# Performance work log

Measured on AMD Instinct MI355X. Metric: run time of the kernel, lower is better.

Reference implementation:

```python
import jax, jax.numpy as jnp
import numpy as np

N_NODES = 200000  # graph size
D = 128           # feature dim == out_size
N1 = 81920        # layer-1 node set size
B = 8192          # batch size
K = 10            # num_sample neighbors


def setup_inputs() -> dict:
    key = jax.random.key(0)
    k = jax.random.split(key, 7)
    raw_features = jax.random.normal(k[0], (N_NODES, D), dtype=jnp.float32)
    # xavier-like scale for weights [out, 2*in]
    W1 = jax.random.normal(k[1], (D, 2 * D), dtype=jnp.float32) * (1.0 / np.sqrt(2 * D))
    W2 = jax.random.normal(k[2], (D, 2 * D), dtype=jnp.float32) * (1.0 / np.sqrt(2 * D))
    layer1_nodes = jax.random.randint(k[3], (N1,), 0, N_NODES)
    neigh0_idx = jax.random.randint(k[4], (N1, K), 0, N_NODES)
    map_batch = jax.random.randint(k[5], (B,), 0, N1)
    neigh1_idx = jax.random.randint(k[6], (B, K), 0, N1)
    return {
        "raw_features": raw_features,
        "W1": W1,
        "W2": W2,
        "layer1_nodes": layer1_nodes,
        "neigh0_idx": neigh0_idx,
        "map_batch": map_batch,
        "neigh1_idx": neigh1_idx,
    }


def _sage_layer(self_feats, agg_feats, W):
    # combined = cat([self, agg], dim=1); relu(W @ combined.T).T == relu(combined @ W.T)
    combined = jnp.concatenate([self_feats, agg_feats], axis=1)
    return jax.nn.relu(combined @ W.T)


def reference(raw_features, W1, W2, layer1_nodes, neigh0_idx, map_batch, neigh1_idx):
    # Layer 1: aggregate raw features over K sampled neighbors (MEAN), gcn=False
    agg0 = jnp.mean(raw_features[neigh0_idx], axis=1)        # [N1, D]
    self0 = raw_features[layer1_nodes]                        # [N1, D]
    h1 = _sage_layer(self0, agg0, W1)                         # [N1, D]
    # Layer 2: aggregate layer-1 embeddings for the batch nodes
    agg1 = jnp.mean(h1[neigh1_idx], axis=1)                   # [B, D]
    self1 = h1[map_batch]                                     # [B, D]
    h2 = _sage_layer(self1, agg1, W2)                         # [B, D]
    return h2
```

## Files before the change

### kernel.cpp

```cpp
#include <hip/hip_runtime.h>
#include <stdint.h>

#define D 128
#define K_NEI 10
#define TILE_M 64

typedef __bf16 bf16x8 __attribute__((ext_vector_type(8)));
typedef float f32x4 __attribute__((ext_vector_type(4)));

__device__ __forceinline__ uint32_t f2bf(float f) {
    union { float f; uint32_t u; } v; v.f = f;
    uint32_t u = v.u;
    return (u + 0x7FFFu + ((u >> 16) & 1u)) >> 16;
}
__device__ __forceinline__ float bf2f(uint32_t h) {
    union { uint32_t u; float f; } v; v.u = h << 16; return v.f;
}
__device__ __forceinline__ uint32_t pack2(float a, float b) {
    return f2bf(a) | (f2bf(b) << 16);
}
__device__ __forceinline__ bf16x8 u4_as_bf16x8(uint4 u) {
    union { uint4 u; bf16x8 b; } v; v.u = u; return v.b;
}

__device__ __forceinline__ uint2 cvt4(f32x4 v) {
    union { __bf16 b[4]; uint2 u; } o;
    o.b[0] = (__bf16)v[0]; o.b[1] = (__bf16)v[1];
    o.b[2] = (__bf16)v[2]; o.b[3] = (__bf16)v[3];
    return o.u;
}
__device__ __forceinline__ bf16x8 cvt8(f32x4 lo, f32x4 hi) {
    union { __bf16 b[8]; bf16x8 v; } o;
    o.b[0] = (__bf16)lo[0]; o.b[1] = (__bf16)lo[1];
    o.b[2] = (__bf16)lo[2]; o.b[3] = (__bf16)lo[3];
    o.b[4] = (__bf16)hi[0]; o.b[5] = (__bf16)hi[1];
    o.b[6] = (__bf16)hi[2]; o.b[7] = (__bf16)hi[3];
    return o.v;
}

__global__ void convert_W2(const float* __restrict__ Wa, const float* __restrict__ Wb_in,
                           uint16_t* __restrict__ Oa, uint16_t* __restrict__ Ob)
{
    const float* W = (blockIdx.x < 16) ? Wa : Wb_in;
    uint16_t*    O = (blockIdx.x < 16) ? Oa : Ob;
    int t = (blockIdx.x & 15) * 256 + threadIdx.x;
    int c = t >> 4, j = t & 15;
    const float* src = W + (size_t)(c & 127) * 256 + (c >> 7) * 128 + j * 8;
    f32x4 a = *(const f32x4*)src;
    f32x4 b = *(const f32x4*)(src + 4);
    uint4 o;
    o.x = pack2(a[0], a[1]); o.y = pack2(a[2], a[3]);
    o.z = pack2(b[0], b[1]); o.w = pack2(b[2], b[3]);
    *(uint4*)(O + (size_t)c * 128 + j * 8) = o;
}

template <bool A_F32>
__global__ __launch_bounds__(256, 2)
void gemm_rw(const void* __restrict__ Asrc_,
             const uint16_t* __restrict__ Wb,
             uint16_t* __restrict__ P, int M)
{
    const int tid  = threadIdx.x;
    const int wave = tid >> 6;
    const int lane = tid & 63;
    const int r16  = lane & 15;
    const int q    = lane >> 4;
    const int h    = wave & 1;

    const int nTiles = M >> 4;
    const int stride = gridDim.x * 2;
    int tile = blockIdx.x * 2 + (wave >> 1);
    if (tile >= nTiles) return;

    bf16x8 Bf[8][4];
    {
        const uint16_t* wb = Wb + (size_t)(h * 128 + r16) * 128 + q * 8;
        #pragma unroll
        for (int nt = 0; nt < 8; ++nt)
            #pragma unroll
            for (int ks = 0; ks < 4; ++ks)
                Bf[nt][ks] = *(const bf16x8*)(wb + nt * 16 * 128 + ks * 32);
    }

    f32x4 preF[8];  uint4 preB[4];

    if (A_F32) {
        const float* row = (const float*)Asrc_ + (size_t)(tile * 16 + r16) * D + q * 8;
        #pragma unroll
        for (int ks = 0; ks < 4; ++ks) {
            preF[2 * ks]     = *(const f32x4*)(row + ks * 32);
            preF[2 * ks + 1] = *(const f32x4*)(row + ks * 32 + 4);
        }
    } else {
        const uint16_t* row = (const uint16_t*)Asrc_ + (size_t)(tile * 16 + r16) * D + q * 8;
        #pragma unroll
        for (int ks = 0; ks < 4; ++ks)
            preB[ks] = *(const uint4*)(row + ks * 32);
    }

    while (tile < nTiles) {
        const int nxt = tile + stride;

        bf16x8 a[4];
        if (A_F32) {
            #pragma unroll
            for (int ks = 0; ks < 4; ++ks)
                a[ks] = cvt8(preF[2 * ks], preF[2 * ks + 1]);
        } else {
            #pragma unroll
            for (int ks = 0; ks < 4; ++ks) a[ks] = u4_as_bf16x8(preB[ks]);
        }

        if (nxt < nTiles) {
            if (A_F32) {
                const float* row = (const float*)Asrc_ + (size_t)(nxt * 16 + r16) * D + q * 8;
                #pragma unroll
                for (int ks = 0; ks < 4; ++ks) {
                    preF[2 * ks]     = *(const f32x4*)(row + ks * 32);
                    preF[2 * ks + 1] = *(const f32x4*)(row + ks * 32 + 4);
                }
            } else {
                const uint16_t* row = (const uint16_t*)Asrc_ + (size_t)(nxt * 16 + r16) * D + q * 8;
                #pragma unroll
                for (int ks = 0; ks < 4; ++ks)
                    preB[ks] = *(const uint4*)(row + ks * 32);
            }
        }

        f32x4 acc[8];
        #pragma unroll
        for (int nt = 0; nt < 8; ++nt) acc[nt] = (f32x4){0.f, 0.f, 0.f, 0.f};

        #pragma unroll
        for (int ks = 0; ks < 4; ++ks)
            #pragma unroll
            for (int nt = 0; nt < 8; ++nt)
                acc[nt] = __builtin_amdgcn_mfma_f32_16x16x32_bf16(Bf[nt][ks], a[ks], acc[nt], 0, 0, 0);

        uint16_t* dst = P + (size_t)(tile * 16 + r16) * 256 + h * 128 + q * 4;
        #pragma unroll
        for (int nt = 0; nt < 8; ++nt)
            *(uint2*)(dst + nt * 16) = cvt4(acc[nt]);

        tile = nxt;
    }
}

template <bool OUT_F32>
__global__ void combine(const uint16_t* __restrict__ P,
                        const int* __restrict__ self_idx,
                        const int* __restrict__ neigh_idx,
                        void* __restrict__ out_, int M)
{
    const int t = blockIdx.x * 256 + threadIdx.x;
    const int i = t >> 4;
    const int j = t & 15;
    if (i >= M) return;

    uint4 sv = *(const uint4*)(P + (size_t)self_idx[i] * 256 + j * 8);

    const int2* nrow2 = (const int2*)(neigh_idx + (size_t)i * K_NEI);
    int idx[K_NEI];
    #pragma unroll
    for (int k = 0; k < 5; ++k) {
        int2 p = nrow2[k];
        idx[2 * k] = p.x; idx[2 * k + 1] = p.y;
    }

    float s0=0,s1=0,s2=0,s3=0,s4=0,s5=0,s6=0,s7=0;
    #pragma unroll
    for (int k = 0; k < K_NEI; ++k) {
        uint4 v = *(const uint4*)(P + (size_t)idx[k] * 256 + 128 + j * 8);
        s0 += bf2f(v.x & 0xFFFFu); s1 += bf2f(v.x >> 16);
        s2 += bf2f(v.y & 0xFFFFu); s3 += bf2f(v.y >> 16);
        s4 += bf2f(v.z & 0xFFFFu); s5 += bf2f(v.z >> 16);
        s6 += bf2f(v.w & 0xFFFFu); s7 += bf2f(v.w >> 16);
    }
    const float inv = 0.1f;
    float r0 = bf2f(sv.x & 0xFFFFu) + s0 * inv, r1 = bf2f(sv.x >> 16) + s1 * inv;
    float r2 = bf2f(sv.y & 0xFFFFu) + s2 * inv, r3 = bf2f(sv.y >> 16) + s3 * inv;
    float r4 = bf2f(sv.z & 0xFFFFu) + s4 * inv, r5 = bf2f(sv.z >> 16) + s5 * inv;
    float r6 = bf2f(sv.w & 0xFFFFu) + s6 * inv, r7 = bf2f(sv.w >> 16) + s7 * inv;
    r0 = r0 > 0.f ? r0 : 0.f; r1 = r1 > 0.f ? r1 : 0.f;
    r2 = r2 > 0.f ? r2 : 0.f; r3 = r3 > 0.f ? r3 : 0.f;
    r4 = r4 > 0.f ? r4 : 0.f; r5 = r5 > 0.f ? r5 : 0.f;
    r6 = r6 > 0.f ? r6 : 0.f; r7 = r7 > 0.f ? r7 : 0.f;

    if (OUT_F32) {
        float* dst = (float*)out_ + (size_t)i * D + j * 8;
        *(f32x4*)dst       = (f32x4){r0, r1, r2, r3};
        *(f32x4*)(dst + 4) = (f32x4){r4, r5, r6, r7};
    } else {
        uint4 o;
        o.x = pack2(r0, r1); o.y = pack2(r2, r3);
        o.z = pack2(r4, r5); o.w = pack2(r6, r7);
        *(uint4*)((uint16_t*)out_ + (size_t)i * D + j * 8) = o;
    }
}

template <bool FEATS_F32, bool OUT_F32>
__global__ void sage_layer(const void* __restrict__ feats_,
                           const float* __restrict__ W,
                           const int* __restrict__ self_idx,
                           const int* __restrict__ neigh_idx,
                           void* __restrict__ out_)
{
    __shared__ __align__(16) uint16_t Alds[TILE_M * 128];
    __shared__ __align__(16) uint16_t Wlds[128 * 128];

    const int tid  = threadIdx.x;
    const int wave = tid >> 6;
    const int lane = tid & 63;
    const int r16  = lane & 15;
    const int q    = lane >> 4;
    const int G    = blockIdx.x * TILE_M;

    const float*    feats_f = (const float*)feats_;
    const uint16_t* feats_b = (const uint16_t*)feats_;

    f32x4 acc[8];
    #pragma unroll
    for (int nt = 0; nt < 8; ++nt) acc[nt] = (f32x4){0.f, 0.f, 0.f, 0.f};

    for (int half = 0; half < 2; ++half) {
        #pragma unroll
        for (int it = 0; it < 8; ++it) {
            int t = it * 256 + tid;
            int j = t >> 4, c = t & 15;
            const float* src = W + (size_t)j * 256 + half * 128 + c * 8;
            f32x4 w0 = *(const f32x4*)(src);
            f32x4 w1 = *(const f32x4*)(src + 4);
            uint4 o;
            o.x = pack2(w0[0], w0[1]); o.y = pack2(w0[2], w0[3]);
            o.z = pack2(w1[0], w1[1]); o.w = pack2(w1[2], w1[3]);
            int cs = c ^ (j & 15);
            *(uint4*)(Wlds + j * 128 + cs * 8) = o;
        }
        if (half == 0) {
            #pragma unroll
            for (int it = 0; it < 4; ++it) {
                int t = it * 256 + tid;
                int n = t >> 4, c = t & 15;
                int node = self_idx[G + n];
                uint4 o;
                if (FEATS_F32) {
                    const float* src = feats_f + (size_t)node * D + c * 8;
                    f32x4 f0 = *(const f32x4*)(src);
                    f32x4 f1 = *(const f32x4*)(src + 4);
                    o.x = pack2(f0[0], f0[1]); o.y = pack2(f0[2], f0[3]);
                    o.z = pack2(f1[0], f1[1]); o.w = pack2(f1[2], f1[3]);
                } else {
                    o = *(const uint4*)(feats_b + (size_t)node * D + c * 8);
                }
                int cs = c ^ (n & 15);
                *(uint4*)(Alds + n * 128 + cs * 8) = o;
            }
        } else {
            #pragma unroll
            for (int it = 0; it < 4; ++it) {
                int t = it * 256 + tid;
                int n = t >> 4, c = t & 15;
                const int* nrow = neigh_idx + (size_t)(G + n) * K_NEI;
                float s0=0,s1=0,s2=0,s3=0,s4=0,s5=0,s6=0,s7=0;
                #pragma unroll
                for (int k = 0; k < K_NEI; ++k) {
                    if (FEATS_F32) {
                        const float* src = feats_f + (size_t)nrow[k] * D + c * 8;
                        f32x4 f0 = *(const f32x4*)(src);
                        f32x4 f1 = *(const f32x4*)(src + 4);
                        s0 += f0[0]; s1 += f0[1]; s2 += f0[2]; s3 += f0[3];
                        s4 += f1[0]; s5 += f1[1]; s6 += f1[2]; s7 += f1[3];
                    } else {
                        uint4 v = *(const uint4*)(feats_b + (size_t)nrow[k] * D + c * 8);
                        s0 += bf2f(v.x & 0xFFFFu); s1 += bf2f(v.x >> 16);
                        s2 += bf2f(v.y & 0xFFFFu); s3 += bf2f(v.y >> 16);
                        s4 += bf2f(v.z & 0xFFFFu); s5 += bf2f(v.z >> 16);
                        s6 += bf2f(v.w & 0xFFFFu); s7 += bf2f(v.w >> 16);
                    }
                }
                const float inv = 0.1f;
                uint4 o;
                o.x = pack2(s0 * inv, s1 * inv);
                o.y = pack2(s2 * inv, s3 * inv);
                o.z = pack2(s4 * inv, s5 * inv);
                o.w = pack2(s6 * inv, s7 * inv);
                int cs = c ^ (n & 15);
                *(uint4*)(Alds + n * 128 + cs * 8) = o;
            }
        }
        __syncthreads();

        #pragma unroll
        for (int ks = 0; ks < 4; ++ks) {
            int cidx = ks * 4 + q;
            bf16x8 a = *(const bf16x8*)(Alds + (wave * 16 + r16) * 128 + ((cidx ^ r16) * 8));
            bf16x8 b[8];
            #pragma unroll
            for (int nt = 0; nt < 8; ++nt) {
                int jj = nt * 16 + r16;
                b[nt] = *(const bf16x8*)(Wlds + jj * 128 + ((cidx ^ r16) * 8));
            }
            #pragma unroll
            for (int nt = 0; nt < 8; ++nt)
                acc[nt] = __builtin_amdgcn_mfma_f32_16x16x32_bf16(a, b[nt], acc[nt], 0, 0, 0);
        }
        __syncthreads();
    }

    const int row_base = G + wave * 16 + q * 4;
    #pragma unroll
    for (int nt = 0; nt < 8; ++nt) {
        int col = nt * 16 + r16;
        #pragma unroll
        for (int r = 0; r < 4; ++r) {
            float v = acc[nt][r];
            v = v > 0.f ? v : 0.f;
            if (OUT_F32) ((float*)out_)[(size_t)(row_base + r) * D + col] = v;
            else ((uint16_t*)out_)[(size_t)(row_base + r) * D + col] = (uint16_t)f2bf(v);
        }
    }
}

extern "C" void kernel_launch(void* const* d_in, const int* in_sizes, int n_in,
                              void* d_out, int out_size, void* d_ws, size_t ws_size,
                              hipStream_t stream) {
    const float* raw = (const float*)d_in[0];
    const float* W1  = (const float*)d_in[1];
    const float* W2  = (const float*)d_in[2];
    const int* layer1_nodes = (const int*)d_in[3];
    const int* neigh0       = (const int*)d_in[4];
    const int* map_batch    = (const int*)d_in[5];
    const int* neigh1       = (const int*)d_in[6];

    const int N_NODES = in_sizes[0] / D;
    const int N1 = in_sizes[3];
    const int B  = in_sizes[5];

    const size_t szP  = (size_t)N_NODES * 256 * 2;
    const size_t szQ  = (size_t)N1 * 256 * 2;
    const size_t szH1 = (size_t)N1 * 128 * 2;
    const size_t szW  = 256 * 128 * 2;
    const size_t needA = (szP > szQ ? szP : szQ) + szH1 + 2 * szW;

    if (ws_size >= needA && (N_NODES % 16) == 0 && (N1 % 16) == 0 && (B % 16) == 0) {
        uint16_t* Pbuf = (uint16_t*)d_ws;
        uint16_t* h1   = (uint16_t*)((char*)d_ws + (szP > szQ ? szP : szQ));
        uint16_t* W1b  = h1 + (size_t)N1 * 128;
        uint16_t* W2b  = W1b + 256 * 128;

        convert_W2<<<32, 256, 0, stream>>>(W1, W2, W1b, W2b);

        gemm_rw<true ><<<512, 256, 0, stream>>>(raw, W1b, Pbuf, N_NODES);

        combine<false><<<(N1 * 16 + 255) / 256, 256, 0, stream>>>(Pbuf, layer1_nodes, neigh0, h1, N1);

        gemm_rw<false><<<512, 256, 0, stream>>>(h1, W2b, Pbuf, N1);

        combine<true ><<<(B * 16 + 255) / 256, 256, 0, stream>>>(Pbuf, map_batch, neigh1, d_out, B);
        return;
    }

    uint16_t* h1 = (uint16_t*)d_ws;
    sage_layer<true,  false><<<N1 / TILE_M, 256, 0, stream>>>(raw, W1, layer1_nodes, neigh0, h1);
    sage_layer<false, true ><<<B  / TILE_M, 256, 0, stream>>>(h1,  W2, map_batch,    neigh1, d_out);
}
```

Before: 251.4 us.

## Gather-then-GEMM: aggregate raw features before projecting instead of projecting all nodes

Replaces the project-all-nodes-then-gather scheme with gather-first. For each layer a gather kernel builds a concatenated [self, mean-neighbor] bf16 row, then a K=256 MFMA GEMM with fused ReLU produces the layer output. This removes the GEMM over all 200k graph nodes and its large intermediate write, which was mostly wasted because only about 81,920 rows are needed. In exchange, the layer-1 gather reads fp32 raw rows, which costs more bytes per gathered row, and it writes an extra concatenated buffer.

```diff
diff --git a/kernel.cpp b/kernel.cpp
--- a/kernel.cpp
+++ b/kernel.cpp
@@ -22,43 +22,92 @@
 __device__ __forceinline__ bf16x8 u4_as_bf16x8(uint4 u) {
     union { uint4 u; bf16x8 b; } v; v.u = u; return v.b;
 }
-
 __device__ __forceinline__ uint2 cvt4(f32x4 v) {
     union { __bf16 b[4]; uint2 u; } o;
     o.b[0] = (__bf16)v[0]; o.b[1] = (__bf16)v[1];
     o.b[2] = (__bf16)v[2]; o.b[3] = (__bf16)v[3];
     return o.u;
 }
-__device__ __forceinline__ bf16x8 cvt8(f32x4 lo, f32x4 hi) {
-    union { __bf16 b[8]; bf16x8 v; } o;
-    o.b[0] = (__bf16)lo[0]; o.b[1] = (__bf16)lo[1];
-    o.b[2] = (__bf16)lo[2]; o.b[3] = (__bf16)lo[3];
-    o.b[4] = (__bf16)hi[0]; o.b[5] = (__bf16)hi[1];
-    o.b[6] = (__bf16)hi[2]; o.b[7] = (__bf16)hi[3];
-    return o.v;
-}
-
-__global__ void convert_W2(const float* __restrict__ Wa, const float* __restrict__ Wb_in,
-                           uint16_t* __restrict__ Oa, uint16_t* __restrict__ Ob)
+
+__global__ void convert_Wc(const float* __restrict__ W1, const float* __restrict__ W2,
+                           uint16_t* __restrict__ O1, uint16_t* __restrict__ O2)
 {
-    const float* W = (blockIdx.x < 16) ? Wa : Wb_in;
-    uint16_t*    O = (blockIdx.x < 16) ? Oa : Ob;
+    const float* W = (blockIdx.x < 16) ? W1 : W2;
+    uint16_t*    O = (blockIdx.x < 16) ? O1 : O2;
     int t = (blockIdx.x & 15) * 256 + threadIdx.x;
-    int c = t >> 4, j = t & 15;
-    const float* src = W + (size_t)(c & 127) * 256 + (c >> 7) * 128 + j * 8;
+    const float* src = W + (size_t)t * 8;
     f32x4 a = *(const f32x4*)src;
     f32x4 b = *(const f32x4*)(src + 4);
     uint4 o;
-    o.x = pack2(a[0], a[1]); o.y = pack2(a[2], a[3]);
-    o.z = pack2(b[0], b[1]); o.w = pack2(b[2], b[3]);
-    *(uint4*)(O + (size_t)c * 128 + j * 8) = o;
-}
-
-template <bool A_F32>
-__global__ __launch_bounds__(256, 2)
-void gemm_rw(const void* __restrict__ Asrc_,
-             const uint16_t* __restrict__ Wb,
-             uint16_t* __restrict__ P, int M)
+    o.x = cvt4(a).x; o.y = cvt4(a).y;
+    o.z = cvt4(b).x; o.w = cvt4(b).y;
+    *(uint4*)(O + (size_t)t * 8) = o;
+}
+
+template <bool SRC_F32>
+__global__ void gather_agg(const void* __restrict__ src_,
+                           const int* __restrict__ self_idx,
+                           const int* __restrict__ neigh_idx,
+                           uint16_t* __restrict__ C, int M)
+{
+    const int t = blockIdx.x * 256 + threadIdx.x;
+    const int i = t >> 4;
+    const int j = t & 15;
+    if (i >= M) return;
+
+    const int2* nrow2 = (const int2*)(neigh_idx + (size_t)i * K_NEI);
+    int idx[K_NEI];
+    #pragma unroll
+    for (int k = 0; k < 5; ++k) {
+        int2 p = nrow2[k];
+        idx[2 * k] = p.x; idx[2 * k + 1] = p.y;
+    }
+    const int self = self_idx[i];
+    uint16_t* c = C + (size_t)i * 256;
+
+    if (SRC_F32) {
+        const float* src = (const float*)src_;
+        const float* srow = src + (size_t)self * D;
+        f32x4 sv0 = *(const f32x4*)(srow + j * 4);
+        f32x4 sv1 = *(const f32x4*)(srow + 64 + j * 4);
+        f32x4 s0 = (f32x4){0.f,0.f,0.f,0.f};
+        f32x4 s1 = (f32x4){0.f,0.f,0.f,0.f};
+        #pragma unroll
+        for (int k = 0; k < K_NEI; ++k) {
+            const float* r = src + (size_t)idx[k] * D;
+            s0 += *(const f32x4*)(r + j * 4);
+            s1 += *(const f32x4*)(r + 64 + j * 4);
+        }
+        *(uint2*)(c + j * 4)       = cvt4(sv0);
+        *(uint2*)(c + 64 + j * 4)  = cvt4(sv1);
+        *(uint2*)(c + 128 + j * 4) = cvt4(s0 * 0.1f);
+        *(uint2*)(c + 192 + j * 4) = cvt4(s1 * 0.1f);
+    } else {
+        const uint16_t* src = (const uint16_t*)src_;
+        uint4 sv = *(const uint4*)(src + (size_t)self * D + j * 8);
+        float s0=0,s1=0,s2=0,s3=0,s4=0,s5=0,s6=0,s7=0;
+        #pragma unroll
+        for (int k = 0; k < K_NEI; ++k) {
+            uint4 v = *(const uint4*)(src + (size_t)idx[k] * D + j * 8);
+            s0 += bf2f(v.x & 0xFFFFu); s1 += bf2f(v.x >> 16);
+            s2 += bf2f(v.y & 0xFFFFu); s3 += bf2f(v.y >> 16);
+            s4 += bf2f(v.z & 0xFFFFu); s5 += bf2f(v.z >> 16);
+            s6 += bf2f(v.w & 0xFFFFu); s7 += bf2f(v.w >> 16);
+        }
+        *(uint4*)(c + j * 8) = sv;
+        const float inv = 0.1f;
+        uint4 o;
+        o.x = pack2(s0 * inv, s1 * inv); o.y = pack2(s2 * inv, s3 * inv);
+        o.z = pack2(s4 * inv, s5 * inv); o.w = pack2(s6 * inv, s7 * inv);
+        *(uint4*)(c + 128 + j * 8) = o;
+    }
+}
+
+template <bool OUT_F32>
+__global__ __launch_bounds__(256)
+void gemm_k256(const uint16_t* __restrict__ A,
+               const uint16_t* __restrict__ Wc,
+               void* __restrict__ out_, int M)
 {
     const int tid  = threadIdx.x;
     const int wave = tid >> 6;
@@ -72,129 +121,61 @@
     int tile = blockIdx.x * 2 + (wave >> 1);
     if (tile >= nTiles) return;
 
-    bf16x8 Bf[8][4];
+    bf16x8 Wf[4][8];
     {
-        const uint16_t* wb = Wb + (size_t)(h * 128 + r16) * 128 + q * 8;
-        #pragma unroll
-        for (int nt = 0; nt < 8; ++nt)
-            #pragma unroll
-            for (int ks = 0; ks < 4; ++ks)
-                Bf[nt][ks] = *(const bf16x8*)(wb + nt * 16 * 128 + ks * 32);
-    }
-
-    f32x4 preF[8];  uint4 preB[4];
-
-    if (A_F32) {
-        const float* row = (const float*)Asrc_ + (size_t)(tile * 16 + r16) * D + q * 8;
-        #pragma unroll
-        for (int ks = 0; ks < 4; ++ks) {
-            preF[2 * ks]     = *(const f32x4*)(row + ks * 32);
-            preF[2 * ks + 1] = *(const f32x4*)(row + ks * 32 + 4);
-        }
-    } else {
-        const uint16_t* row = (const uint16_t*)Asrc_ + (size_t)(tile * 16 + r16) * D + q * 8;
-        #pragma unroll
-        for (int ks = 0; ks < 4; ++ks)
-            preB[ks] = *(const uint4*)(row + ks * 32);
+        const uint16_t* wb = Wc + (size_t)(h * 64 + r16) * 256 + q * 8;
+        #pragma unroll
+        for (int nt = 0; nt < 4; ++nt)
+            #pragma unroll
+            for (int ks = 0; ks < 8; ++ks)
+                Wf[nt][ks] = *(const bf16x8*)(wb + nt * 16 * 256 + ks * 32);
+    }
+
+    uint4 preB[8];
+    {
+        const uint16_t* row = A + (size_t)(tile * 16 + r16) * 256 + q * 8;
+        #pragma unroll
+        for (int ks = 0; ks < 8; ++ks) preB[ks] = *(const uint4*)(row + ks * 32);
     }
 
     while (tile < nTiles) {
         const int nxt = tile + stride;
 
-        bf16x8 a[4];
-        if (A_F32) {
-            #pragma unroll
-            for (int ks = 0; ks < 4; ++ks)
-                a[ks] = cvt8(preF[2 * ks], preF[2 * ks + 1]);
-        } else {
-            #pragma unroll
-            for (int ks = 0; ks < 4; ++ks) a[ks] = u4_as_bf16x8(preB[ks]);
-        }
+        bf16x8 a[8];
+        #pragma unroll
+        for (int ks = 0; ks < 8; ++ks) a[ks] = u4_as_bf16x8(preB[ks]);
 
         if (nxt < nTiles) {
-            if (A_F32) {
-                const float* row = (const float*)Asrc_ + (size_t)(nxt * 16 + r16) * D + q * 8;
-                #pragma unroll
-                for (int ks = 0; ks < 4; ++ks) {
-                    preF[2 * ks]     = *(const f32x4*)(row + ks * 32);
-                    preF[2 * ks + 1] = *(const f32x4*)(row + ks * 32 + 4);
-                }
-            } else {
-                const uint16_t* row = (const uint16_t*)Asrc_ + (size_t)(nxt * 16 + r16) * D + q * 8;
-                #pragma unroll
-                for (int ks = 0; ks < 4; ++ks)
-                    preB[ks] = *(const uint4*)(row + ks * 32);
-            }
-        }
-
-        f32x4 acc[8];
-        #pragma unroll
-        for (int nt = 0; nt < 8; ++nt) acc[nt] = (f32x4){0.f, 0.f, 0.f, 0.f};
-
-        #pragma unroll
-        for (int ks = 0; ks < 4; ++ks)
-            #pragma unroll
-            for (int nt = 0; nt < 8; ++nt)
-                acc[nt] = __builtin_amdgcn_mfma_f32_16x16x32_bf16(Bf[nt][ks], a[ks], acc[nt], 0, 0, 0);
-
-        uint16_t* dst = P + (size_t)(tile * 16 + r16) * 256 + h * 128 + q * 4;
-        #pragma unroll
-        for (int nt = 0; nt < 8; ++nt)
-            *(uint2*)(dst + nt * 16) = cvt4(acc[nt]);
-
+            const uint16_t* row = A + (size_t)(nxt * 16 + r16) * 256 + q * 8;
+            #pragma unroll
+            for (int ks = 0; ks < 8; ++ks) preB[ks] = *(const uint4*)(row + ks * 32);
+        }
+
+        f32x4 acc[4];
+        #pragma unroll
+        for (int nt = 0; nt < 4; ++nt) acc[nt] = (f32x4){0.f,0.f,0.f,0.f};
+
+        #pragma unroll
+        for (int ks = 0; ks < 8; ++ks)
+            #pragma unroll
+            for (int nt = 0; nt < 4; ++nt)
+                acc[nt] = __builtin_amdgcn_mfma_f32_16x16x32_bf16(Wf[nt][ks], a[ks], acc[nt], 0, 0, 0);
+
+        const size_t row = (size_t)(tile * 16 + r16);
+        const int col0 = h * 64 + q * 4;
+        #pragma unroll
+        for (int nt = 0; nt < 4; ++nt) {
+            f32x4 v = acc[nt];
+            v[0] = v[0] > 0.f ? v[0] : 0.f;
+            v[1] = v[1] > 0.f ? v[1] : 0.f;
+            v[2] = v[2] > 0.f ? v[2] : 0.f;
+            v[3] = v[3] > 0.f ? v[3] : 0.f;
+            if (OUT_F32)
+                *(f32x4*)((float*)out_ + row * 128 + col0 + nt * 16) = v;
+            else
+                *(uint2*)((uint16_t*)out_ + row * 128 + col0 + nt * 16) = cvt4(v);
+        }
         tile = nxt;
-    }
-}
-
-template <bool OUT_F32>
-__global__ void combine(const uint16_t* __restrict__ P,
-                        const int* __restrict__ self_idx,
-                        const int* __restrict__ neigh_idx,
-                        void* __restrict__ out_, int M)
-{
-    const int t = blockIdx.x * 256 + threadIdx.x;
-    const int i = t >> 4;
-    const int j = t & 15;
-    if (i >= M) return;
-
-    uint4 sv = *(const uint4*)(P + (size_t)self_idx[i] * 256 + j * 8);
-
-    const int2* nrow2 = (const int2*)(neigh_idx + (size_t)i * K_NEI);
-    int idx[K_NEI];
-    #pragma unroll
-    for (int k = 0; k < 5; ++k) {
-        int2 p = nrow2[k];
-        idx[2 * k] = p.x; idx[2 * k + 1] = p.y;
-    }
-
-    float s0=0,s1=0,s2=0,s3=0,s4=0,s5=0,s6=0,s7=0;
-    #pragma unroll
-    for (int k = 0; k < K_NEI; ++k) {
-        uint4 v = *(const uint4*)(P + (size_t)idx[k] * 256 + 128 + j * 8);
-        s0 += bf2f(v.x & 0xFFFFu); s1 += bf2f(v.x >> 16);
-        s2 += bf2f(v.y & 0xFFFFu); s3 += bf2f(v.y >> 16);
-        s4 += bf2f(v.z & 0xFFFFu); s5 += bf2f(v.z >> 16);
-        s6 += bf2f(v.w & 0xFFFFu); s7 += bf2f(v.w >> 16);
-    }
-    const float inv = 0.1f;
-    float r0 = bf2f(sv.x & 0xFFFFu) + s0 * inv, r1 = bf2f(sv.x >> 16) + s1 * inv;
-    float r2 = bf2f(sv.y & 0xFFFFu) + s2 * inv, r3 = bf2f(sv.y >> 16) + s3 * inv;
-    float r4 = bf2f(sv.z & 0xFFFFu) + s4 * inv, r5 = bf2f(sv.z >> 16) + s5 * inv;
-    float r6 = bf2f(sv.w & 0xFFFFu) + s6 * inv, r7 = bf2f(sv.w >> 16) + s7 * inv;
-    r0 = r0 > 0.f ? r0 : 0.f; r1 = r1 > 0.f ? r1 : 0.f;
-    r2 = r2 > 0.f ? r2 : 0.f; r3 = r3 > 0.f ? r3 : 0.f;
-    r4 = r4 > 0.f ? r4 : 0.f; r5 = r5 > 0.f ? r5 : 0.f;
-    r6 = r6 > 0.f ? r6 : 0.f; r7 = r7 > 0.f ? r7 : 0.f;
-
-    if (OUT_F32) {
-        float* dst = (float*)out_ + (size_t)i * D + j * 8;
-        *(f32x4*)dst       = (f32x4){r0, r1, r2, r3};
-        *(f32x4*)(dst + 4) = (f32x4){r4, r5, r6, r7};
-    } else {
-        uint4 o;
-        o.x = pack2(r0, r1); o.y = pack2(r2, r3);
-        o.z = pack2(r4, r5); o.w = pack2(r6, r7);
-        *(uint4*)((uint16_t*)out_ + (size_t)i * D + j * 8) = o;
     }
 }
 
@@ -332,31 +313,33 @@
     const int* map_batch    = (const int*)d_in[5];
     const int* neigh1       = (const int*)d_in[6];
 
-    const int N_NODES = in_sizes[0] / D;
     const int N1 = in_sizes[3];
     const int B  = in_sizes[5];
 
-    const size_t szP  = (size_t)N_NODES * 256 * 2;
-    const size_t szQ  = (size_t)N1 * 256 * 2;
+    const size_t szC1 = (size_t)N1 * 256 * 2;
     const size_t szH1 = (size_t)N1 * 128 * 2;
-    const size_t szW  = 256 * 128 * 2;
-    const size_t needA = (szP > szQ ? szP : szQ) + szH1 + 2 * szW;
-
-    if (ws_size >= needA && (N_NODES % 16) == 0 && (N1 % 16) == 0 && (B % 16) == 0) {
-        uint16_t* Pbuf = (uint16_t*)d_ws;
-        uint16_t* h1   = (uint16_t*)((char*)d_ws + (szP > szQ ? szP : szQ));
-        uint16_t* W1b  = h1 + (size_t)N1 * 128;
-        uint16_t* W2b  = W1b + 256 * 128;
-
-        convert_W2<<<32, 256, 0, stream>>>(W1, W2, W1b, W2b);
-
-        gemm_rw<true ><<<512, 256, 0, stream>>>(raw, W1b, Pbuf, N_NODES);
-
-        combine<false><<<(N1 * 16 + 255) / 256, 256, 0, stream>>>(Pbuf, layer1_nodes, neigh0, h1, N1);
-
-        gemm_rw<false><<<512, 256, 0, stream>>>(h1, W2b, Pbuf, N1);
-
-        combine<true ><<<(B * 16 + 255) / 256, 256, 0, stream>>>(Pbuf, map_batch, neigh1, d_out, B);
+    const size_t szC2 = (size_t)B * 256 * 2;
+    const size_t szW  = 128 * 256 * 2;
+    const size_t need = szC1 + szH1 + szC2 + 2 * szW;
+
+    if (ws_size >= need && (N1 % 16) == 0 && (B % 16) == 0) {
+        uint16_t* C1  = (uint16_t*)d_ws;
+        uint16_t* h1  = C1 + (size_t)N1 * 256;
+        uint16_t* C2  = h1 + (size_t)N1 * 128;
+        uint16_t* W1c = C2 + (size_t)B * 256;
+        uint16_t* W2c = W1c + 128 * 256;
+
+        convert_Wc<<<32, 256, 0, stream>>>(W1, W2, W1c, W2c);
+
+        gather_agg<true ><<<(N1 * 16 + 255) / 256, 256, 0, stream>>>(raw, layer1_nodes, neigh0, C1, N1);
+
+        int g1 = (N1 / 16 + 1) / 2; if (g1 > 512) g1 = 512;
+        gemm_k256<false><<<g1, 256, 0, stream>>>(C1, W1c, h1, N1);
+
+        gather_agg<false><<<(B * 16 + 255) / 256, 256, 0, stream>>>(h1, map_batch, neigh1, C2, B);
+
+        int g2 = (B / 16 + 1) / 2; if (g2 > 512) g2 = 512;
+        gemm_k256<true ><<<g2, 256, 0, stream>>>(C2, W2c, d_out, B);
         return;
     }
 
```

Result: faster. 236.1 us (-6.1%).
